# Performance work log

Measured on AMD Instinct MI355X. Metric: run time of the kernel, lower is better.

Reference implementation:

```python
import jax, jax.numpy as jnp
import numpy as np

D, H, K = 384, 6, 8

def _ln(x, g, b, eps=1e-5):
    mu = jnp.mean(x, axis=-1, keepdims=True)
    var = jnp.mean((x - mu) ** 2, axis=-1, keepdims=True)
    return (x - mu) * jax.lax.rsqrt(var + eps) * g + b

def setup_inputs() -> dict:
    key = jax.random.key(0)
    ks = jax.random.split(key, 20)
    B, N = 4, 2048
    s = 0.02
    inp = {
        'x': jax.random.normal(ks[0], (B, N, D), jnp.float32),
        'knn_index': jax.random.randint(ks[1], (B * K * N,), 0, B * N, jnp.int64),
        'ln1_g': jnp.ones((D,), jnp.float32),
        'ln1_b': jnp.zeros((D,), jnp.float32),
        'w_qkv': jax.random.normal(ks[2], (D, 3 * D), jnp.float32) * s,
        'w_proj': jax.random.normal(ks[3], (D, D), jnp.float32) * s,
        'b_proj': jnp.zeros((D,), jnp.float32),
        'w_knn': jax.random.normal(ks[4], (2 * D, D), jnp.float32) * s,
        'b_knn': jnp.zeros((D,), jnp.float32),
        'w_g1': jax.random.normal(ks[5], (2 * D, D), jnp.float32) * s,
        'b_g1': jnp.zeros((D,), jnp.float32),
        'w_g2': jax.random.normal(ks[6], (D, D), jnp.float32) * s,
        'b_g2': jnp.zeros((D,), jnp.float32),
        'ln2_g': jnp.ones((D,), jnp.float32),
        'ln2_b': jnp.zeros((D,), jnp.float32),
        'w_fc1': jax.random.normal(ks[7], (D, 4 * D), jnp.float32) * s,
        'b_fc1': jnp.zeros((4 * D,), jnp.float32),
        'w_fc2': jax.random.normal(ks[8], (4 * D, D), jnp.float32) * s,
        'b_fc2': jnp.zeros((D,), jnp.float32),
    }
    return inp

def reference(x, knn_index, ln1_g, ln1_b, w_qkv, w_proj, b_proj, w_knn, b_knn,
              w_g1, b_g1, w_g2, b_g2, ln2_g, ln2_b, w_fc1, b_fc1, w_fc2, b_fc2):
    B, N, _ = x.shape
    hd = D // H
    scale = hd ** -0.5
    nx = _ln(x, ln1_g, ln1_b)
    # --- self attention ---
    qkv = (nx @ w_qkv).reshape(B, N, 3, H, hd).transpose(2, 0, 3, 1, 4)  # [3,B,H,N,hd]
    q, k, v = qkv[0], qkv[1], qkv[2]
    attn = jax.nn.softmax(jnp.einsum('bhnd,bhmd->bhnm', q * scale, k), axis=-1)
    attn_out = jnp.einsum('bhnm,bhmd->bhnd', attn, v).transpose(0, 2, 1, 3).reshape(B, N, D)
    attn_out = attn_out @ w_proj + b_proj
    # --- EdgeConv-style graph feature: gather-concat-MLP-maxpool ---
    feat = nx.reshape(B * N, D)[knn_index].reshape(B, K, N, D)
    xe = jnp.broadcast_to(nx[:, None], (B, K, N, D))
    gf = jnp.concatenate([feat - xe, xe], axis=-1)  # [B,K,N,2D]
    knn_out = jnp.max(jax.nn.leaky_relu(gf @ w_knn + b_knn, 0.2), axis=1)  # [B,N,D]
    # --- salience gate ---
    gi = jnp.concatenate([attn_out, knn_out], axis=-1)
    gate = jax.nn.sigmoid(jax.nn.gelu(gi @ w_g1 + b_g1, approximate=False) @ w_g2 + b_g2)
    fused = (1 - gate) * attn_out + gate * knn_out
    x = x + fused
    # --- FFN ---
    h = jax.nn.gelu(_ln(x, ln2_g, ln2_b) @ w_fc1 + b_fc1, approximate=False)
    x = x + (h @ w_fc2 + b_fc2)
    return x
```

## Files before the change

kernel.cpp:

```cpp
#include <hip/hip_runtime.h>
#include <math.h>

typedef unsigned short u16;
typedef __attribute__((ext_vector_type(8))) short short8;
typedef __attribute__((ext_vector_type(4))) float floatx4;
typedef __attribute__((ext_vector_type(4))) short sh4v;

union sh4u { sh4v v; u16 u[4]; };
union sh8u { short8 v; u16 u[8]; };

__device__ __forceinline__ floatx4 mfma16(short8 a, short8 b, floatx4 c) {
  return __builtin_amdgcn_mfma_f32_16x16x32_bf16(a, b, c, 0, 0, 0);
}

__device__ __forceinline__ floatx4 zero4() {
  floatx4 z = {0.f, 0.f, 0.f, 0.f};
  return z;
}

__device__ __forceinline__ u16 f2b(float f) {
  union { float f; unsigned u; } v; v.f = f;
  unsigned u = v.u;
  return (u16)((u + 0x7FFFu + ((u >> 16) & 1u)) >> 16);
}

__device__ __forceinline__ float b2f(u16 u) {
  union { unsigned u; float f; } v; v.u = ((unsigned)u) << 16;
  return v.f;
}

__device__ __forceinline__ float gelu_exact(float x) {
  return 0.5f * x * (1.f + erff(x * 0.70710678118654752440f));
}

__device__ __forceinline__ unsigned pack2(float a, float b) {
  return (unsigned)f2b(a) | ((unsigned)f2b(b) << 16);
}

__device__ __forceinline__ unsigned permpack(float p0, float p1) {
  return __builtin_amdgcn_perm(__float_as_uint(p1), __float_as_uint(p0), 0x07060302u);
}

__global__ __launch_bounds__(256) void tcln_kernel(
    const float* __restrict__ p0, const float* __restrict__ p1,
    const float* __restrict__ p2, const float* __restrict__ p3,
    const float* __restrict__ p4, const float* __restrict__ p5,
    const float* __restrict__ wknn,
    u16* __restrict__ o0, u16* __restrict__ o1, u16* __restrict__ o2,
    u16* __restrict__ o3, u16* __restrict__ o4, u16* __restrict__ o5,
    u16* __restrict__ wcT,
    const float* __restrict__ x, const float* __restrict__ g,
    const float* __restrict__ bia, u16* __restrict__ nx) {
  __shared__ u16 L[64][66];
  int t = blockIdx.x, tid = threadIdx.x;
  if (t >= 612) {
    int wave = tid >> 6, lane = tid & 63;
    int row = (t - 612) * 4 + wave;
    const float* xr = x + (size_t)row * 384;
    float v[6];
    float s = 0.f;
#pragma unroll
    for (int j = 0; j < 6; j++) { v[j] = xr[lane + 64 * j]; s += v[j]; }
#pragma unroll
    for (int off = 32; off > 0; off >>= 1) s += __shfl_xor(s, off);
    float mu = s * (1.f / 384.f);
    float ss = 0.f;
#pragma unroll
    for (int j = 0; j < 6; j++) { float d = v[j] - mu; ss += d * d; }
#pragma unroll
    for (int off = 32; off > 0; off >>= 1) ss += __shfl_xor(ss, off);
    float rstd = rsqrtf(ss * (1.f / 384.f) + 1e-5f);
    u16* orow = nx + (size_t)row * 384;
#pragma unroll
    for (int j = 0; j < 6; j++) {
      int d = lane + 64 * j;
      orow[d] = f2b((v[j] - mu) * rstd * g[d] + bia[d]);
    }
    return;
  }
  if (t >= 540) {
    t -= 540;
    int tk = t / 12, tn = t % 12;
    int k0 = tk * 64, j0 = tn * 64;
#pragma unroll
    for (int i = 0; i < 4; i++) {
      int c = tid + 256 * i;
      int r = c >> 4, c4 = (c & 15) * 4;
      floatx4 v;
      if (j0 < 384) {
        v = *(const floatx4*)(wknn + (size_t)(k0 + r) * 384 + j0 + c4);
      } else {
        floatx4 a = *(const floatx4*)(wknn + (size_t)(384 + k0 + r) * 384 + (j0 - 384) + c4);
        floatx4 b = *(const floatx4*)(wknn + (size_t)(k0 + r) * 384 + (j0 - 384) + c4);
        v = a - b;
      }
      *(unsigned*)&L[r][c4]     = pack2(v[0], v[1]);
      *(unsigned*)&L[r][c4 + 2] = pack2(v[2], v[3]);
    }
    __syncthreads();
#pragma unroll
    for (int i = 0; i < 2; i++) {
      int c = tid + 256 * i;
      int nn = c >> 3, k8 = (c & 7) * 8;
      sh8u pk;
#pragma unroll
      for (int j = 0; j < 8; j++) pk.u[j] = L[k8 + j][nn];
      *(short8*)(wcT + (size_t)(j0 + nn) * 384 + k0 + k8) = pk.v;
    }
    return;
  }
  const float* src; u16* dst; int Kd, Nd, tk, tn;
  if      (t < 108) { src = p0; dst = o0; Kd = 384;  Nd = 1152; tk = t / 18; tn = t % 18; }
  else if (t < 144) { src = p1; dst = o1; Kd = 384;  Nd = 384;  t -= 108; tk = t / 6;  tn = t % 6; }
  else if (t < 216) { src = p2; dst = o2; Kd = 768;  Nd = 384;  t -= 144; tk = t / 6;  tn = t % 6; }
  else if (t < 252) { src = p3; dst = o3; Kd = 384;  Nd = 384;  t -= 216; tk = t / 6;  tn = t % 6; }
  else if (t < 396) { src = p4; dst = o4; Kd = 384;  Nd = 1536; t -= 252; tk = t / 24; tn = t % 24; }
  else              { src = p5; dst = o5; Kd = 1536; Nd = 384;  t -= 396; tk = t / 6;  tn = t % 6; }
  int k0 = tk * 64, n0 = tn * 64;
#pragma unroll
  for (int i = 0; i < 4; i++) {
    int c = tid + 256 * i;
    int r = c >> 4, c4 = (c & 15) * 4;
    floatx4 v = *(const floatx4*)(src + (size_t)(k0 + r) * Nd + n0 + c4);
    *(unsigned*)&L[r][c4]     = pack2(v[0], v[1]);
    *(unsigned*)&L[r][c4 + 2] = pack2(v[2], v[3]);
  }
  __syncthreads();
#pragma unroll
  for (int i = 0; i < 2; i++) {
    int c = tid + 256 * i;
    int nn = c >> 3, k8 = (c & 7) * 8;
    sh8u pk;
#pragma unroll
    for (int j = 0; j < 8; j++) pk.u[j] = L[k8 + j][nn];
    *(short8*)(dst + (size_t)(n0 + nn) * Kd + k0 + k8) = pk.v;
  }
}

__global__ __launch_bounds__(256) void lnb_kernel(const u16* __restrict__ x,
                                                  const float* __restrict__ g,
                                                  const float* __restrict__ bia,
                                                  u16* __restrict__ out) {
  int wave = threadIdx.x >> 6, lane = threadIdx.x & 63;
  int row = blockIdx.x * 4 + wave;
  const u16* xr = x + (size_t)row * 384;
  float v[6];
  float s = 0.f;
#pragma unroll
  for (int j = 0; j < 6; j++) { v[j] = b2f(xr[lane + 64 * j]); s += v[j]; }
#pragma unroll
  for (int off = 32; off > 0; off >>= 1) s += __shfl_xor(s, off);
  float mu = s * (1.f / 384.f);
  float ss = 0.f;
#pragma unroll
  for (int j = 0; j < 6; j++) { float d = v[j] - mu; ss += d * d; }
#pragma unroll
  for (int off = 32; off > 0; off >>= 1) ss += __shfl_xor(ss, off);
  float rstd = rsqrtf(ss * (1.f / 384.f) + 1e-5f);
  u16* orow = out + (size_t)row * 384;
#pragma unroll
  for (int j = 0; j < 6; j++) {
    int d = lane + 64 * j;
    orow[d] = f2b((v[j] - mu) * rstd * g[d] + bia[d]);
  }
}

template <int EPI>
__global__ __launch_bounds__(256) void gemm64_kernel(
    const u16* __restrict__ A0, const u16* __restrict__ A1, int Ksplit,
    const u16* __restrict__ BwT, const u16* __restrict__ BwT2, int N, int K,
    const float* __restrict__ bias,
    float* __restrict__ outF, u16* __restrict__ outB, u16* __restrict__ outB2,
    const u16* __restrict__ eA16, const u16* __restrict__ eK16,
    const float* __restrict__ eX, u16* __restrict__ outV) {
  __shared__ u16 As[64][72];
  __shared__ u16 Bs[128][72];
  int tid = threadIdx.x;
  int lane = tid & 63, w = tid >> 6, quad = lane >> 4, l16 = lane & 15;
  int n0 = blockIdx.x * 128, m0 = blockIdx.y * 64;
  int ra = tid >> 3, ca = (tid & 7) * 8;
  const u16* Bsrc = BwT;
  int nbase = n0;
  if (EPI == 8 && n0 >= 1152) { Bsrc = BwT2; nbase = n0 - 1152; }
  floatx4 acc[4][2];
#pragma unroll
  for (int i = 0; i < 4; i++)
#pragma unroll
    for (int j = 0; j < 2; j++) acc[i][j] = zero4();

  short8 pa[2], pb[4];
  auto loadAB = [&](int k0) {
    const u16* Ap;
    int kk, sA;
    if (k0 < Ksplit) { Ap = A0; kk = k0; sA = Ksplit; }
    else             { Ap = A1; kk = k0 - Ksplit; sA = K - Ksplit; }
    pa[0] = *(const short8*)(Ap + (size_t)(m0 + ra) * sA + kk + ca);
    pa[1] = *(const short8*)(Ap + (size_t)(m0 + ra + 32) * sA + kk + ca);
#pragma unroll
    for (int i = 0; i < 4; i++)
      pb[i] = *(const short8*)(Bsrc + (size_t)(nbase + ra + 32 * i) * K + k0 + ca);
  };
  loadAB(0);
  int iters = K >> 6;
  for (int kt = 0; kt < iters; kt++) {
    __syncthreads();
    *(short8*)&As[ra][ca] = pa[0];
    *(short8*)&As[ra + 32][ca] = pa[1];
#pragma unroll
    for (int i = 0; i < 4; i++) *(short8*)&Bs[ra + 32 * i][ca] = pb[i];
    __syncthreads();
    if (kt + 1 < iters) loadAB((kt + 1) * 64);
#pragma unroll
    for (int kh = 0; kh < 2; kh++) {
      short8 af[4], bfr[2];
#pragma unroll
      for (int mt = 0; mt < 4; mt++)
        af[mt] = *(const short8*)&As[mt * 16 + l16][kh * 32 + quad * 8];
#pragma unroll
      for (int nt = 0; nt < 2; nt++)
        bfr[nt] = *(const short8*)&Bs[w * 32 + nt * 16 + l16][kh * 32 + quad * 8];
#pragma unroll
      for (int mt = 0; mt < 4; mt++)
#pragma unroll
        for (int nt = 0; nt < 2; nt++)
          acc[mt][nt] = mfma16(af[mt], bfr[nt], acc[mt][nt]);
    }
  }

#pragma unroll
  for (int mt = 0; mt < 4; mt++)
#pragma unroll
    for (int nt = 0; nt < 2; nt++) {
      int col = n0 + w * 32 + nt * 16 + l16;
      int row0 = m0 + mt * 16 + quad * 4;
      if (EPI == 8) {
        if (col < 1152) {
          float sc = (col < 384) ? 0.18033688011112042f : 1.f;
          sh4u pk;
#pragma unroll
          for (int r = 0; r < 4; r++) {
            u16 bv = f2b(acc[mt][nt][r] * sc);
            outB[(size_t)(row0 + r) * 1152 + col] = bv;
            pk.u[r] = bv;
          }
          if (col >= 768) {
            int b = row0 >> 11, n = row0 & 2047;
            int hd = col - 768;
            *(sh4v*)(outV + ((size_t)(b * 6 + (hd >> 6)) * 64 + (hd & 63)) * 2048 + n) = pk.v;
          }
        } else {
#pragma unroll
          for (int r = 0; r < 4; r++)
            outB2[(size_t)(row0 + r) * 768 + (col - 1152)] = f2b(acc[mt][nt][r]);
        }
      } else {
#pragma unroll
        for (int r = 0; r < 4; r++) {
          size_t rc = (size_t)(row0 + r) * N + col;
          float v = acc[mt][nt][r];
          if (EPI == 3) {
            outB[rc] = f2b(gelu_exact(v + bias[col]));
          } else if (EPI == 4) {
            float gte = 1.f / (1.f + __expf(-(v + bias[col])));
            float fu = (1.f - gte) * b2f(eA16[rc]) + gte * b2f(eK16[rc]);
            outB[rc] = f2b(eX[rc] + fu);
          } else if (EPI == 7) {
            outF[rc] = v + bias[col] + b2f(eA16[rc]);
          }
        }
      }
    }
}

__global__ __launch_bounds__(256) void attnknn_kernel(
    const u16* __restrict__ qkv, const u16* __restrict__ Vt,
    u16* __restrict__ OPb, float* __restrict__ LS,
    const u16* __restrict__ GBb, const int* __restrict__ kidx,
    const float* __restrict__ bknn, u16* __restrict__ knn_bf) {
  __shared__ u16 Ks[64][72];
  __shared__ u16 Vts[64][72];
  __shared__ u16 Ps[4][32][72];
  int bid = blockIdx.x, tid = threadIdx.x;
  int lane = tid & 63, w = tid >> 6, quad = lane >> 4, l16 = lane & 15;
  if (bid >= 1536) {
    int row = (bid - 1536) * 4 + w;
    int b = row >> 11, n = row & 2047;
    float base[6], acc[6];
#pragma unroll
    for (int j = 0; j < 6; j++) {
      int d = lane + 64 * j;
      base[j] = b2f(GBb[(size_t)row * 768 + 384 + d]) + bknn[d];
      acc[j] = -1e30f;
    }
    for (int kk = 0; kk < 8; kk++) {
      int g = kidx[(b * 8 + kk) * 2048 + n];
      const u16* Gr = GBb + (size_t)g * 768;
#pragma unroll
      for (int j = 0; j < 6; j++) {
        float v = b2f(Gr[lane + 64 * j]) + base[j];
        v = v > 0.f ? v : 0.2f * v;
        acc[j] = fmaxf(acc[j], v);
      }
    }
#pragma unroll
    for (int j = 0; j < 6; j++)
      knn_bf[(size_t)row * 384 + lane + 64 * j] = f2b(acc[j]);
    return;
  }
  int split = bid / 384;
  int rr = bid - split * 384;
  int bh = rr >> 4, b = bh / 6, h = bh % 6;
  int q0 = (rr & 15) * 128;
  const u16* qbase = qkv + (size_t)b * 2048 * 1152 + h * 64;
  const u16* kbase = qbase + 384 + (size_t)split * 512 * 1152;
  const u16* vtb = Vt + (size_t)bh * 64 * 2048 + split * 512;
  short8 qf[2][2];
#pragma unroll
  for (int s = 0; s < 2; s++) {
    int qrow = q0 + w * 32 + s * 16 + l16;
    qf[s][0] = *(const short8*)(qbase + (size_t)qrow * 1152 + quad * 8);
    qf[s][1] = *(const short8*)(qbase + (size_t)qrow * 1152 + 32 + quad * 8);
  }
  short8 ones;
#pragma unroll
  for (int j = 0; j < 8; j++) ones[j] = (short)0x3F80;
  floatx4 O[4][2];
  floatx4 accL[2] = {zero4(), zero4()};
#pragma unroll
  for (int i = 0; i < 4; i++)
#pragma unroll
    for (int s = 0; s < 2; s++) O[i][s] = zero4();

  int rb = tid >> 3, c8 = (tid & 7) * 8;
  short8 rk[2], rv[2];
  rk[0] = *(const short8*)(kbase + (size_t)rb * 1152 + c8);
  rk[1] = *(const short8*)(kbase + (size_t)(rb + 32) * 1152 + c8);
  rv[0] = *(const short8*)(vtb + (size_t)rb * 2048 + c8);
  rv[1] = *(const short8*)(vtb + (size_t)(rb + 32) * 2048 + c8);

  for (int kt = 0; kt < 8; kt++) {
    __syncthreads();
    *(short8*)&Ks[rb][c8] = rk[0];
    *(short8*)&Ks[rb + 32][c8] = rk[1];
    *(short8*)&Vts[rb][c8] = rv[0];
    *(short8*)&Vts[rb + 32][c8] = rv[1];
    __syncthreads();
    if (kt < 7) {
      int key0 = (kt + 1) * 64;
      rk[0] = *(const short8*)(kbase + (size_t)(key0 + rb) * 1152 + c8);
      rk[1] = *(const short8*)(kbase + (size_t)(key0 + rb + 32) * 1152 + c8);
      rv[0] = *(const short8*)(vtb + (size_t)rb * 2048 + key0 + c8);
      rv[1] = *(const short8*)(vtb + (size_t)(rb + 32) * 2048 + key0 + c8);
    }
#pragma unroll
    for (int mt = 0; mt < 4; mt++) {
      short8 k0 = *(const short8*)&Ks[mt * 16 + l16][quad * 8];
      short8 k1 = *(const short8*)&Ks[mt * 16 + l16][32 + quad * 8];
#pragma unroll
      for (int s = 0; s < 2; s++) {
        floatx4 st = mfma16(k0, qf[s][0], zero4());
        st = mfma16(k1, qf[s][1], st);
        uint2 pk;
        pk.x = permpack(exp2f(st[0]), exp2f(st[1]));
        pk.y = permpack(exp2f(st[2]), exp2f(st[3]));
        *(uint2*)&Ps[w][s * 16 + l16][mt * 16 + quad * 4] = pk;
      }
    }
    short8 pf[2][2];
#pragma unroll
    for (int s = 0; s < 2; s++) {
      pf[s][0] = *(const short8*)&Ps[w][s * 16 + l16][quad * 8];
      pf[s][1] = *(const short8*)&Ps[w][s * 16 + l16][32 + quad * 8];
      accL[s] = mfma16(ones, pf[s][0], accL[s]);
      accL[s] = mfma16(ones, pf[s][1], accL[s]);
    }
#pragma unroll
    for (int mt2 = 0; mt2 < 4; mt2++) {
      short8 v0 = *(const short8*)&Vts[mt2 * 16 + l16][quad * 8];
      short8 v1 = *(const short8*)&Vts[mt2 * 16 + l16][32 + quad * 8];
#pragma unroll
      for (int s = 0; s < 2; s++) {
        O[mt2][s] = mfma16(v0, pf[s][0], O[mt2][s]);
        O[mt2][s] = mfma16(v1, pf[s][1], O[mt2][s]);
      }
    }
  }
#pragma unroll
  for (int s = 0; s < 2; s++) {
    int row = b * 2048 + q0 + w * 32 + s * 16 + l16;
    u16* orow = OPb + (size_t)split * 8192 * 384 + (size_t)row * 384 + h * 64;
#pragma unroll
    for (int mt2 = 0; mt2 < 4; mt2++) {
      sh4u pk;
#pragma unroll
      for (int r = 0; r < 4; r++) pk.u[r] = f2b(O[mt2][s][r]);
      *(sh4v*)(orow + mt2 * 16 + quad * 4) = pk.v;
    }
    if (quad == 0) LS[split * 8192 + row] = accL[s][0];
  }
}

__global__ __launch_bounds__(256) void projc_kernel(
    const u16* __restrict__ OPb, const float* __restrict__ LS,
    const u16* __restrict__ BwT, const float* __restrict__ bias,
    u16* __restrict__ outB) {
  __shared__ u16 As[64][72];
  __shared__ u16 Bs[128][72];
  int tid = threadIdx.x;
  int lane = tid & 63, w = tid >> 6, quad = lane >> 4, l16 = lane & 15;
  int n0 = blockIdx.x * 128, m0 = blockIdx.y * 64;
  int ra = tid >> 3, ca = (tid & 7) * 8;
  const size_t SP = (size_t)8192 * 384;
  floatx4 acc[4][2];
#pragma unroll
  for (int i = 0; i < 4; i++)
#pragma unroll
    for (int j = 0; j < 2; j++) acc[i][j] = zero4();

  short8 pa[2], pb[4];
  auto loadAB = [&](int k0) {
#pragma unroll
    for (int i = 0; i < 2; i++) {
      const u16* p = OPb + (size_t)(m0 + ra + 32 * i) * 384 + k0 + ca;
      sh8u a0, a1, a2, a3, pk;
      a0.v = *(const short8*)p;
      a1.v = *(const short8*)(p + SP);
      a2.v = *(const short8*)(p + 2 * SP);
      a3.v = *(const short8*)(p + 3 * SP);
#pragma unroll
      for (int j = 0; j < 8; j++)
        pk.u[j] = f2b((b2f(a0.u[j]) + b2f(a1.u[j])) + (b2f(a2.u[j]) + b2f(a3.u[j])));
      pa[i] = pk.v;
    }
#pragma unroll
    for (int i = 0; i < 4; i++)
      pb[i] = *(const short8*)(BwT + (size_t)(n0 + ra + 32 * i) * 384 + k0 + ca);
  };
  loadAB(0);
  for (int kt = 0; kt < 6; kt++) {
    __syncthreads();
    *(short8*)&As[ra][ca] = pa[0];
    *(short8*)&As[ra + 32][ca] = pa[1];
#pragma unroll
    for (int i = 0; i < 4; i++) *(short8*)&Bs[ra + 32 * i][ca] = pb[i];
    __syncthreads();
    if (kt < 5) loadAB((kt + 1) * 64);
#pragma unroll
    for (int kh = 0; kh < 2; kh++) {
      short8 af[4], bfr[2];
#pragma unroll
      for (int mt = 0; mt < 4; mt++)
        af[mt] = *(const short8*)&As[mt * 16 + l16][kh * 32 + quad * 8];
#pragma unroll
      for (int nt = 0; nt < 2; nt++)
        bfr[nt] = *(const short8*)&Bs[w * 32 + nt * 16 + l16][kh * 32 + quad * 8];
#pragma unroll
      for (int mt = 0; mt < 4; mt++)
#pragma unroll
        for (int nt = 0; nt < 2; nt++)
          acc[mt][nt] = mfma16(af[mt], bfr[nt], acc[mt][nt]);
    }
  }
#pragma unroll
  for (int mt = 0; mt < 4; mt++) {
    int row0 = m0 + mt * 16 + quad * 4;
    float rl[4];
#pragma unroll
    for (int r = 0; r < 4; r++) {
      int gr = row0 + r;
      rl[r] = 1.f / ((LS[gr] + LS[8192 + gr]) + (LS[16384 + gr] + LS[24576 + gr]));
    }
#pragma unroll
    for (int nt = 0; nt < 2; nt++) {
      int col = n0 + w * 32 + nt * 16 + l16;
#pragma unroll
      for (int r = 0; r < 4; r++)
        outB[(size_t)(row0 + r) * 384 + col] = f2b(acc[mt][nt][r] * rl[r] + bias[col]);
    }
  }
}

extern "C" void kernel_launch(void* const* d_in, const int* in_sizes, int n_in,
                              void* d_out, int out_size, void* d_ws, size_t ws_size,
                              hipStream_t stream) {
  const float* x    = (const float*)d_in[0];
  const int* kidx   = (const int*)d_in[1];
  const float* ln1g = (const float*)d_in[2];
  const float* ln1b = (const float*)d_in[3];
  const float* wqkv = (const float*)d_in[4];
  const float* wproj= (const float*)d_in[5];
  const float* bproj= (const float*)d_in[6];
  const float* wknn = (const float*)d_in[7];
  const float* bknn = (const float*)d_in[8];
  const float* wg1  = (const float*)d_in[9];
  const float* bg1  = (const float*)d_in[10];
  const float* wg2  = (const float*)d_in[11];
  const float* bg2  = (const float*)d_in[12];
  const float* ln2g = (const float*)d_in[13];
  const float* ln2b = (const float*)d_in[14];
  const float* wfc1 = (const float*)d_in[15];
  const float* bfc1 = (const float*)d_in[16];
  const float* wfc2 = (const float*)d_in[17];
  const float* bfc2 = (const float*)d_in[18];
  float* out = (float*)d_out;

  const int M = 8192;
  char* ws = (char*)d_ws;
  size_t off = 0;
  auto alloc = [&](size_t bytes) -> char* {
    char* p = ws + off;
    off += (bytes + 255) & ~(size_t)255;
    return p;
  };
  u16* nx_bf    = (u16*)alloc((size_t)M * 384 * 2);
  u16* qkv_bf   = (u16*)alloc((size_t)M * 1152 * 2);
  u16* attn_bf  = (u16*)alloc((size_t)M * 384 * 2);
  u16* GBb      = (u16*)alloc((size_t)M * 768 * 2);
  u16* knn_bf   = (u16*)alloc((size_t)M * 384 * 2);
  u16* x2b      = (u16*)alloc((size_t)M * 384 * 2);
  u16* t1_bf    = (u16*)alloc((size_t)M * 384 * 2);
  u16* nx2_bf   = (u16*)alloc((size_t)M * 384 * 2);
  u16* Vt_b     = (u16*)alloc((size_t)24 * 64 * 2048 * 2);
  u16* OPb      = (u16*)alloc((size_t)4 * M * 384 * 2);
  float* LS     = (float*)alloc((size_t)4 * M * 4);
  u16* wqkvT    = (u16*)alloc((size_t)1152 * 384 * 2);
  u16* wprojT   = (u16*)alloc(384 * 384 * 2);
  u16* wcT      = (u16*)alloc((size_t)768 * 384 * 2);
  u16* wg1T     = (u16*)alloc((size_t)384 * 768 * 2);
  u16* wg2T     = (u16*)alloc(384 * 384 * 2);
  u16* wfc1T    = (u16*)alloc((size_t)1536 * 384 * 2);
  u16* wfc2T    = (u16*)alloc((size_t)384 * 1536 * 2);
  u16* h_bf     = qkv_bf;

  tcln_kernel<<<2660, 256, 0, stream>>>(wqkv, wproj, wg1, wg2, wfc1, wfc2, wknn,
                                        wqkvT, wprojT, wg1T, wg2T, wfc1T, wfc2T, wcT,
                                        x, ln1g, ln1b, nx_bf);
  gemm64_kernel<8><<<dim3(15, 128), 256, 0, stream>>>(nx_bf, nx_bf, 384, wqkvT, wcT, 1920, 384,
                                                      nullptr, nullptr, qkv_bf, GBb,
                                                      nullptr, nullptr, nullptr, Vt_b);
  attnknn_kernel<<<3584, 256, 0, stream>>>(qkv_bf, Vt_b, OPb, LS,
                                           GBb, kidx, bknn, knn_bf);
  projc_kernel<<<dim3(3, 128), 256, 0, stream>>>(OPb, LS, wprojT, bproj, attn_bf);
  gemm64_kernel<3><<<dim3(3, 128), 256, 0, stream>>>(attn_bf, knn_bf, 384, wg1T, nullptr, 384, 768,
                                                     bg1, nullptr, t1_bf, nullptr,
                                                     nullptr, nullptr, nullptr, nullptr);
  gemm64_kernel<4><<<dim3(3, 128), 256, 0, stream>>>(t1_bf, t1_bf, 384, wg2T, nullptr, 384, 384,
                                                     bg2, nullptr, x2b, nullptr,
                                                     attn_bf, knn_bf, x, nullptr);
  lnb_kernel<<<2048, 256, 0, stream>>>(x2b, ln2g, ln2b, nx2_bf);
  gemm64_kernel<3><<<dim3(12, 128), 256, 0, stream>>>(nx2_bf, nx2_bf, 384, wfc1T, nullptr, 1536, 384,
                                                      bfc1, nullptr, h_bf, nullptr,
                                                      nullptr, nullptr, nullptr, nullptr);
  gemm64_kernel<7><<<dim3(3, 128), 256, 0, stream>>>(h_bf, h_bf, 1536, wfc2T, nullptr, 384, 1536,
                                                     bfc2, out, nullptr, nullptr,
                                                     x2b, nullptr, nullptr, nullptr);
  (void)in_sizes; (void)n_in; (void)out_size; (void)ws_size;
}
```

Baseline: 278.6 us.

## Use per-GEMM tile sizes: 128x128 for wide GEMMs, 32-row tiles for narrow

Adds a 128x128-tile GEMM kernel, with four waves each owning a 64x64 sub-tile, for the wide QKV/knn and FC1 GEMMs. This raises MFMA work per LDS load and halves the block count. Adds a 32-row tile kernel for the N=384, K=384 projection and gate GEMMs, doubling their block count so the GPU fills better, and folds the split-softmax merge into it in place of the separate projection kernel. The larger tile raises register and LDS use and gives fewer blocks for the wide GEMMs, which may lower occupancy.

```diff
diff --git a/kernel.cpp b/kernel.cpp
--- a/kernel.cpp
+++ b/kernel.cpp
@@ -166,80 +166,76 @@
 }
 
 template <int EPI>
-__global__ __launch_bounds__(256) void gemm64_kernel(
-    const u16* __restrict__ A0, const u16* __restrict__ A1, int Ksplit,
-    const u16* __restrict__ BwT, const u16* __restrict__ BwT2, int N, int K,
-    const float* __restrict__ bias,
-    float* __restrict__ outF, u16* __restrict__ outB, u16* __restrict__ outB2,
-    const u16* __restrict__ eA16, const u16* __restrict__ eK16,
-    const float* __restrict__ eX, u16* __restrict__ outV) {
-  __shared__ u16 As[64][72];
+__global__ __launch_bounds__(256) void gemm128p_kernel(
+    const u16* __restrict__ A0, const u16* __restrict__ BwT,
+    const u16* __restrict__ BwT2, int N, int K,
+    const float* __restrict__ bias, u16* __restrict__ outB, u16* __restrict__ outB2,
+    u16* __restrict__ outV) {
+  __shared__ u16 As[128][72];
   __shared__ u16 Bs[128][72];
   int tid = threadIdx.x;
-  int lane = tid & 63, w = tid >> 6, quad = lane >> 4, l16 = lane & 15;
-  int n0 = blockIdx.x * 128, m0 = blockIdx.y * 64;
+  int lane = tid & 63, wave = tid >> 6, quad = lane >> 4, l16 = lane & 15;
+  int n0 = blockIdx.x * 128, m0 = blockIdx.y * 128;
+  int wm = (wave >> 1) * 64, wn = (wave & 1) * 64;
   int ra = tid >> 3, ca = (tid & 7) * 8;
   const u16* Bsrc = BwT;
   int nbase = n0;
   if (EPI == 8 && n0 >= 1152) { Bsrc = BwT2; nbase = n0 - 1152; }
-  floatx4 acc[4][2];
+  floatx4 acc[4][4];
 #pragma unroll
   for (int i = 0; i < 4; i++)
 #pragma unroll
-    for (int j = 0; j < 2; j++) acc[i][j] = zero4();
-
-  short8 pa[2], pb[4];
+    for (int j = 0; j < 4; j++) acc[i][j] = zero4();
+
+  short8 pa[4], pb[4];
   auto loadAB = [&](int k0) {
-    const u16* Ap;
-    int kk, sA;
-    if (k0 < Ksplit) { Ap = A0; kk = k0; sA = Ksplit; }
-    else             { Ap = A1; kk = k0 - Ksplit; sA = K - Ksplit; }
-    pa[0] = *(const short8*)(Ap + (size_t)(m0 + ra) * sA + kk + ca);
-    pa[1] = *(const short8*)(Ap + (size_t)(m0 + ra + 32) * sA + kk + ca);
-#pragma unroll
-    for (int i = 0; i < 4; i++)
+#pragma unroll
+    for (int i = 0; i < 4; i++) {
+      pa[i] = *(const short8*)(A0 + (size_t)(m0 + ra + 32 * i) * K + k0 + ca);
       pb[i] = *(const short8*)(Bsrc + (size_t)(nbase + ra + 32 * i) * K + k0 + ca);
+    }
   };
   loadAB(0);
   int iters = K >> 6;
   for (int kt = 0; kt < iters; kt++) {
     __syncthreads();
-    *(short8*)&As[ra][ca] = pa[0];
-    *(short8*)&As[ra + 32][ca] = pa[1];
-#pragma unroll
-    for (int i = 0; i < 4; i++) *(short8*)&Bs[ra + 32 * i][ca] = pb[i];
+#pragma unroll
+    for (int i = 0; i < 4; i++) {
+      *(short8*)&As[ra + 32 * i][ca] = pa[i];
+      *(short8*)&Bs[ra + 32 * i][ca] = pb[i];
+    }
     __syncthreads();
     if (kt + 1 < iters) loadAB((kt + 1) * 64);
 #pragma unroll
     for (int kh = 0; kh < 2; kh++) {
-      short8 af[4], bfr[2];
-#pragma unroll
-      for (int mt = 0; mt < 4; mt++)
-        af[mt] = *(const short8*)&As[mt * 16 + l16][kh * 32 + quad * 8];
-#pragma unroll
-      for (int nt = 0; nt < 2; nt++)
-        bfr[nt] = *(const short8*)&Bs[w * 32 + nt * 16 + l16][kh * 32 + quad * 8];
-#pragma unroll
-      for (int mt = 0; mt < 4; mt++)
-#pragma unroll
-        for (int nt = 0; nt < 2; nt++)
-          acc[mt][nt] = mfma16(af[mt], bfr[nt], acc[mt][nt]);
-    }
-  }
-
-#pragma unroll
-  for (int mt = 0; mt < 4; mt++)
-#pragma unroll
-    for (int nt = 0; nt < 2; nt++) {
-      int col = n0 + w * 32 + nt * 16 + l16;
-      int row0 = m0 + mt * 16 + quad * 4;
+      short8 af[4], bfr[4];
+#pragma unroll
+      for (int ti = 0; ti < 4; ti++)
+        af[ti] = *(const short8*)&As[wm + ti * 16 + l16][kh * 32 + quad * 8];
+#pragma unroll
+      for (int tj = 0; tj < 4; tj++)
+        bfr[tj] = *(const short8*)&Bs[wn + tj * 16 + l16][kh * 32 + quad * 8];
+#pragma unroll
+      for (int ti = 0; ti < 4; ti++)
+#pragma unroll
+        for (int tj = 0; tj < 4; tj++)
+          acc[ti][tj] = mfma16(af[ti], bfr[tj], acc[ti][tj]);
+    }
+  }
+
+#pragma unroll
+  for (int ti = 0; ti < 4; ti++)
+#pragma unroll
+    for (int tj = 0; tj < 4; tj++) {
+      int col = n0 + wn + tj * 16 + l16;
+      int row0 = m0 + wm + ti * 16 + quad * 4;
       if (EPI == 8) {
         if (col < 1152) {
           float sc = (col < 384) ? 0.18033688011112042f : 1.f;
           sh4u pk;
 #pragma unroll
           for (int r = 0; r < 4; r++) {
-            u16 bv = f2b(acc[mt][nt][r] * sc);
+            u16 bv = f2b(acc[ti][tj][r] * sc);
             outB[(size_t)(row0 + r) * 1152 + col] = bv;
             pk.u[r] = bv;
           }
@@ -251,25 +247,188 @@
         } else {
 #pragma unroll
           for (int r = 0; r < 4; r++)
-            outB2[(size_t)(row0 + r) * 768 + (col - 1152)] = f2b(acc[mt][nt][r]);
+            outB2[(size_t)(row0 + r) * 768 + (col - 1152)] = f2b(acc[ti][tj][r]);
         }
       } else {
 #pragma unroll
-        for (int r = 0; r < 4; r++) {
-          size_t rc = (size_t)(row0 + r) * N + col;
-          float v = acc[mt][nt][r];
-          if (EPI == 3) {
-            outB[rc] = f2b(gelu_exact(v + bias[col]));
-          } else if (EPI == 4) {
-            float gte = 1.f / (1.f + __expf(-(v + bias[col])));
-            float fu = (1.f - gte) * b2f(eA16[rc]) + gte * b2f(eK16[rc]);
-            outB[rc] = f2b(eX[rc] + fu);
-          } else if (EPI == 7) {
-            outF[rc] = v + bias[col] + b2f(eA16[rc]);
-          }
+        for (int r = 0; r < 4; r++)
+          outB[(size_t)(row0 + r) * N + col] = f2b(gelu_exact(acc[ti][tj][r] + bias[col]));
+      }
+    }
+}
+
+template <int EPI>
+__global__ __launch_bounds__(256) void gemm64_kernel(
+    const u16* __restrict__ A0, const u16* __restrict__ A1, int Ksplit,
+    const u16* __restrict__ BwT, int N, int K,
+    const float* __restrict__ bias,
+    float* __restrict__ outF, u16* __restrict__ outB,
+    const u16* __restrict__ eA16) {
+  __shared__ u16 As[64][72];
+  __shared__ u16 Bs[128][72];
+  int tid = threadIdx.x;
+  int lane = tid & 63, w = tid >> 6, quad = lane >> 4, l16 = lane & 15;
+  int n0 = blockIdx.x * 128, m0 = blockIdx.y * 64;
+  int ra = tid >> 3, ca = (tid & 7) * 8;
+  floatx4 acc[4][2];
+#pragma unroll
+  for (int i = 0; i < 4; i++)
+#pragma unroll
+    for (int j = 0; j < 2; j++) acc[i][j] = zero4();
+
+  short8 pa[2], pb[4];
+  auto loadAB = [&](int k0) {
+    const u16* Ap;
+    int kk, sA;
+    if (k0 < Ksplit) { Ap = A0; kk = k0; sA = Ksplit; }
+    else             { Ap = A1; kk = k0 - Ksplit; sA = K - Ksplit; }
+    pa[0] = *(const short8*)(Ap + (size_t)(m0 + ra) * sA + kk + ca);
+    pa[1] = *(const short8*)(Ap + (size_t)(m0 + ra + 32) * sA + kk + ca);
+#pragma unroll
+    for (int i = 0; i < 4; i++)
+      pb[i] = *(const short8*)(BwT + (size_t)(n0 + ra + 32 * i) * K + k0 + ca);
+  };
+  loadAB(0);
+  int iters = K >> 6;
+  for (int kt = 0; kt < iters; kt++) {
+    __syncthreads();
+    *(short8*)&As[ra][ca] = pa[0];
+    *(short8*)&As[ra + 32][ca] = pa[1];
+#pragma unroll
+    for (int i = 0; i < 4; i++) *(short8*)&Bs[ra + 32 * i][ca] = pb[i];
+    __syncthreads();
+    if (kt + 1 < iters) loadAB((kt + 1) * 64);
+#pragma unroll
+    for (int kh = 0; kh < 2; kh++) {
+      short8 af[4], bfr[2];
+#pragma unroll
+      for (int mt = 0; mt < 4; mt++)
+        af[mt] = *(const short8*)&As[mt * 16 + l16][kh * 32 + quad * 8];
+#pragma unroll
+      for (int nt = 0; nt < 2; nt++)
+        bfr[nt] = *(const short8*)&Bs[w * 32 + nt * 16 + l16][kh * 32 + quad * 8];
+#pragma unroll
+      for (int mt = 0; mt < 4; mt++)
+#pragma unroll
+        for (int nt = 0; nt < 2; nt++)
+          acc[mt][nt] = mfma16(af[mt], bfr[nt], acc[mt][nt]);
+    }
+  }
+
+#pragma unroll
+  for (int mt = 0; mt < 4; mt++)
+#pragma unroll
+    for (int nt = 0; nt < 2; nt++) {
+      int col = n0 + w * 32 + nt * 16 + l16;
+      int row0 = m0 + mt * 16 + quad * 4;
+#pragma unroll
+      for (int r = 0; r < 4; r++) {
+        size_t rc = (size_t)(row0 + r) * N + col;
+        float v = acc[mt][nt][r];
+        if (EPI == 3) {
+          outB[rc] = f2b(gelu_exact(v + bias[col]));
+        } else if (EPI == 7) {
+          outF[rc] = v + bias[col] + b2f(eA16[rc]);
         }
       }
     }
+}
+
+template <int EPI>
+__global__ __launch_bounds__(256) void gemm32_kernel(
+    const u16* __restrict__ A0, const float* __restrict__ LS,
+    const u16* __restrict__ BwT, int N, int K,
+    const float* __restrict__ bias,
+    u16* __restrict__ outB,
+    const u16* __restrict__ eA16, const u16* __restrict__ eK16,
+    const float* __restrict__ eX) {
+  __shared__ u16 As[32][72];
+  __shared__ u16 Bs[128][72];
+  int tid = threadIdx.x;
+  int lane = tid & 63, w = tid >> 6, quad = lane >> 4, l16 = lane & 15;
+  int n0 = blockIdx.x * 128, m0 = blockIdx.y * 32;
+  int ra = tid >> 3, ca = (tid & 7) * 8;
+  const size_t SP = (size_t)8192 * 384;
+  floatx4 acc[2][2];
+#pragma unroll
+  for (int i = 0; i < 2; i++)
+#pragma unroll
+    for (int j = 0; j < 2; j++) acc[i][j] = zero4();
+
+  short8 pa, pb[4];
+  auto loadAB = [&](int k0) {
+    if (EPI == 9) {
+      const u16* p = A0 + (size_t)(m0 + ra) * 384 + k0 + ca;
+      sh8u a0, a1, a2, a3, pk;
+      a0.v = *(const short8*)p;
+      a1.v = *(const short8*)(p + SP);
+      a2.v = *(const short8*)(p + 2 * SP);
+      a3.v = *(const short8*)(p + 3 * SP);
+#pragma unroll
+      for (int j = 0; j < 8; j++)
+        pk.u[j] = f2b((b2f(a0.u[j]) + b2f(a1.u[j])) + (b2f(a2.u[j]) + b2f(a3.u[j])));
+      pa = pk.v;
+    } else {
+      pa = *(const short8*)(A0 + (size_t)(m0 + ra) * K + k0 + ca);
+    }
+#pragma unroll
+    for (int i = 0; i < 4; i++)
+      pb[i] = *(const short8*)(BwT + (size_t)(n0 + ra + 32 * i) * K + k0 + ca);
+  };
+  loadAB(0);
+  int iters = K >> 6;
+  for (int kt = 0; kt < iters; kt++) {
+    __syncthreads();
+    *(short8*)&As[ra][ca] = pa;
+#pragma unroll
+    for (int i = 0; i < 4; i++) *(short8*)&Bs[ra + 32 * i][ca] = pb[i];
+    __syncthreads();
+    if (kt + 1 < iters) loadAB((kt + 1) * 64);
+#pragma unroll
+    for (int kh = 0; kh < 2; kh++) {
+      short8 af[2], bfr[2];
+#pragma unroll
+      for (int mt = 0; mt < 2; mt++)
+        af[mt] = *(const short8*)&As[mt * 16 + l16][kh * 32 + quad * 8];
+#pragma unroll
+      for (int nt = 0; nt < 2; nt++)
+        bfr[nt] = *(const short8*)&Bs[w * 32 + nt * 16 + l16][kh * 32 + quad * 8];
+#pragma unroll
+      for (int mt = 0; mt < 2; mt++)
+#pragma unroll
+        for (int nt = 0; nt < 2; nt++)
+          acc[mt][nt] = mfma16(af[mt], bfr[nt], acc[mt][nt]);
+    }
+  }
+
+#pragma unroll
+  for (int mt = 0; mt < 2; mt++) {
+    int row0 = m0 + mt * 16 + quad * 4;
+    float rl[4];
+    if (EPI == 9) {
+#pragma unroll
+      for (int r = 0; r < 4; r++) {
+        int gr = row0 + r;
+        rl[r] = 1.f / ((LS[gr] + LS[8192 + gr]) + (LS[16384 + gr] + LS[24576 + gr]));
+      }
+    }
+#pragma unroll
+    for (int nt = 0; nt < 2; nt++) {
+      int col = n0 + w * 32 + nt * 16 + l16;
+#pragma unroll
+      for (int r = 0; r < 4; r++) {
+        size_t rc = (size_t)(row0 + r) * N + col;
+        float v = acc[mt][nt][r];
+        if (EPI == 9) {
+          outB[rc] = f2b(v * rl[r] + bias[col]);
+        } else {
+          float gte = 1.f / (1.f + __expf(-(v + bias[col])));
+          float fu = (1.f - gte) * b2f(eA16[rc]) + gte * b2f(eK16[rc]);
+          outB[rc] = f2b(eX[rc] + fu);
+        }
+      }
+    }
+  }
 }
 
 __global__ __launch_bounds__(256) void attnknn_kernel(
@@ -397,86 +556,6 @@
       *(sh4v*)(orow + mt2 * 16 + quad * 4) = pk.v;
     }
     if (quad == 0) LS[split * 8192 + row] = accL[s][0];
-  }
-}
-
-__global__ __launch_bounds__(256) void projc_kernel(
-    const u16* __restrict__ OPb, const float* __restrict__ LS,
-    const u16* __restrict__ BwT, const float* __restrict__ bias,
-    u16* __restrict__ outB) {
-  __shared__ u16 As[64][72];
-  __shared__ u16 Bs[128][72];
-  int tid = threadIdx.x;
-  int lane = tid & 63, w = tid >> 6, quad = lane >> 4, l16 = lane & 15;
-  int n0 = blockIdx.x * 128, m0 = blockIdx.y * 64;
-  int ra = tid >> 3, ca = (tid & 7) * 8;
-  const size_t SP = (size_t)8192 * 384;
-  floatx4 acc[4][2];
-#pragma unroll
-  for (int i = 0; i < 4; i++)
-#pragma unroll
-    for (int j = 0; j < 2; j++) acc[i][j] = zero4();
-
-  short8 pa[2], pb[4];
-  auto loadAB = [&](int k0) {
-#pragma unroll
-    for (int i = 0; i < 2; i++) {
-      const u16* p = OPb + (size_t)(m0 + ra + 32 * i) * 384 + k0 + ca;
-      sh8u a0, a1, a2, a3, pk;
-      a0.v = *(const short8*)p;
-      a1.v = *(const short8*)(p + SP);
-      a2.v = *(const short8*)(p + 2 * SP);
-      a3.v = *(const short8*)(p + 3 * SP);
-#pragma unroll
-      for (int j = 0; j < 8; j++)
-        pk.u[j] = f2b((b2f(a0.u[j]) + b2f(a1.u[j])) + (b2f(a2.u[j]) + b2f(a3.u[j])));
-      pa[i] = pk.v;
-    }
-#pragma unroll
-    for (int i = 0; i < 4; i++)
-      pb[i] = *(const short8*)(BwT + (size_t)(n0 + ra + 32 * i) * 384 + k0 + ca);
-  };
-  loadAB(0);
-  for (int kt = 0; kt < 6; kt++) {
-    __syncthreads();
-    *(short8*)&As[ra][ca] = pa[0];
-    *(short8*)&As[ra + 32][ca] = pa[1];
-#pragma unroll
-    for (int i = 0; i < 4; i++) *(short8*)&Bs[ra + 32 * i][ca] = pb[i];
-    __syncthreads();
-    if (kt < 5) loadAB((kt + 1) * 64);
-#pragma unroll
-    for (int kh = 0; kh < 2; kh++) {
-      short8 af[4], bfr[2];
-#pragma unroll
-      for (int mt = 0; mt < 4; mt++)
-        af[mt] = *(const short8*)&As[mt * 16 + l16][kh * 32 + quad * 8];
-#pragma unroll
-      for (int nt = 0; nt < 2; nt++)
-        bfr[nt] = *(const short8*)&Bs[w * 32 + nt * 16 + l16][kh * 32 + quad * 8];
-#pragma unroll
-      for (int mt = 0; mt < 4; mt++)
-#pragma unroll
-        for (int nt = 0; nt < 2; nt++)
-          acc[mt][nt] = mfma16(af[mt], bfr[nt], acc[mt][nt]);
-    }
-  }
-#pragma unroll
-  for (int mt = 0; mt < 4; mt++) {
-    int row0 = m0 + mt * 16 + quad * 4;
-    float rl[4];
-#pragma unroll
-    for (int r = 0; r < 4; r++) {
-      int gr = row0 + r;
-      rl[r] = 1.f / ((LS[gr] + LS[8192 + gr]) + (LS[16384 + gr] + LS[24576 + gr]));
-    }
-#pragma unroll
-    for (int nt = 0; nt < 2; nt++) {
-      int col = n0 + w * 32 + nt * 16 + l16;
-#pragma unroll
-      for (int r = 0; r < 4; r++)
-        outB[(size_t)(row0 + r) * 384 + col] = f2b(acc[mt][nt][r] * rl[r] + bias[col]);
-    }
   }
 }
 
@@ -535,24 +614,22 @@
   tcln_kernel<<<2660, 256, 0, stream>>>(wqkv, wproj, wg1, wg2, wfc1, wfc2, wknn,
                                         wqkvT, wprojT, wg1T, wg2T, wfc1T, wfc2T, wcT,
                                         x, ln1g, ln1b, nx_bf);
-  gemm64_kernel<8><<<dim3(15, 128), 256, 0, stream>>>(nx_bf, nx_bf, 384, wqkvT, wcT, 1920, 384,
-                                                      nullptr, nullptr, qkv_bf, GBb,
-                                                      nullptr, nullptr, nullptr, Vt_b);
+  gemm128p_kernel<8><<<dim3(15, 64), 256, 0, stream>>>(nx_bf, wqkvT, wcT, 1920, 384,
+                                                       nullptr, qkv_bf, GBb, Vt_b);
   attnknn_kernel<<<3584, 256, 0, stream>>>(qkv_bf, Vt_b, OPb, LS,
                                            GBb, kidx, bknn, knn_bf);
-  projc_kernel<<<dim3(3, 128), 256, 0, stream>>>(OPb, LS, wprojT, bproj, attn_bf);
-  gemm64_kernel<3><<<dim3(3, 128), 256, 0, stream>>>(attn_bf, knn_bf, 384, wg1T, nullptr, 384, 768,
-                                                     bg1, nullptr, t1_bf, nullptr,
-                                                     nullptr, nullptr, nullptr, nullptr);
-  gemm64_kernel<4><<<dim3(3, 128), 256, 0, stream>>>(t1_bf, t1_bf, 384, wg2T, nullptr, 384, 384,
-                                                     bg2, nullptr, x2b, nullptr,
-                                                     attn_bf, knn_bf, x, nullptr);
+  gemm32_kernel<9><<<dim3(3, 256), 256, 0, stream>>>(OPb, LS, wprojT, 384, 384,
+                                                     bproj, attn_bf,
+                                                     nullptr, nullptr, nullptr);
+  gemm64_kernel<3><<<dim3(3, 128), 256, 0, stream>>>(attn_bf, knn_bf, 384, wg1T, 384, 768,
+                                                     bg1, nullptr, t1_bf, nullptr);
+  gemm32_kernel<4><<<dim3(3, 256), 256, 0, stream>>>(t1_bf, nullptr, wg2T, 384, 384,
+                                                     bg2, x2b,
+                                                     attn_bf, knn_bf, x);
   lnb_kernel<<<2048, 256, 0, stream>>>(x2b, ln2g, ln2b, nx2_bf);
-  gemm64_kernel<3><<<dim3(12, 128), 256, 0, stream>>>(nx2_bf, nx2_bf, 384, wfc1T, nullptr, 1536, 384,
-                                                      bfc1, nullptr, h_bf, nullptr,
-                                                      nullptr, nullptr, nullptr, nullptr);
-  gemm64_kernel<7><<<dim3(3, 128), 256, 0, stream>>>(h_bf, h_bf, 1536, wfc2T, nullptr, 384, 1536,
-                                                     bfc2, out, nullptr, nullptr,
-                                                     x2b, nullptr, nullptr, nullptr);
+  gemm128p_kernel<3><<<dim3(12, 64), 256, 0, stream>>>(nx2_bf, wfc1T, nullptr, 1536, 384,
+                                                       bfc1, h_bf, nullptr, nullptr);
+  gemm64_kernel<7><<<dim3(3, 128), 256, 0, stream>>>(h_bf, h_bf, 1536, wfc2T, 384, 1536,
+                                                     bfc2, out, nullptr, x2b);
   (void)in_sizes; (void)n_in; (void)out_size; (void)ws_size;
 }
```

New measurement: 324.1 us. 1.16x slower.
